# Kernel tuning notes

Hardware: AMD Instinct MI355X
Metric: run time of the kernel (lower is better)

## Reference

```python
import jax, jax.numpy as jnp
import numpy as np

N = 50000
E = 1600000
NFEAT = 256
NHID = 256
PAD_N = 60000


def setup_inputs() -> dict:
    key = jax.random.key(0)
    ks = jax.random.split(key, 8)
    x = jax.random.normal(ks[0], (N, NFEAT), dtype=jnp.float32)
    adj_rows = jax.random.randint(ks[1], (E,), 0, N)
    adj_cols = jax.random.randint(ks[2], (E,), 0, N)
    adj_vals = jax.random.uniform(ks[3], (E,), dtype=jnp.float32)
    pos_idx = jnp.arange(N)  # unique rows within padded output
    W1 = jax.random.normal(ks[4], (NFEAT, NHID), dtype=jnp.float32) * 0.05
    b1 = jax.random.normal(ks[5], (NHID,), dtype=jnp.float32) * 0.05
    W2 = jax.random.normal(ks[6], (NHID, NHID), dtype=jnp.float32) * 0.05
    b2 = jax.random.normal(ks[7], (NHID,), dtype=jnp.float32) * 0.05
    return {"x": x, "adj_rows": adj_rows, "adj_cols": adj_cols,
            "adj_vals": adj_vals, "pad_n": PAD_N, "pos_idx": pos_idx,
            "W1": W1, "b1": b1, "W2": W2, "b2": b2}


def _graph_conv(x, rows, cols, vals, W, b):
    # support = x @ W ; out = adj @ support + b  (adj in COO form)
    support = x @ W                                   # [N, H]
    msgs = vals[:, None] * support[cols]              # [E, H] gather + scale
    agg = jax.ops.segment_sum(msgs, rows, num_segments=x.shape[0])
    return agg + b


def reference(x, adj_rows, adj_cols, adj_vals, pad_n, pos_idx, W1, b1, W2, b2):
    h = jax.nn.relu(_graph_conv(x, adj_rows, adj_cols, adj_vals, W1, b1))
    # dropout: eval mode (training=False) -> identity
    h = jax.nn.relu(_graph_conv(h, adj_rows, adj_cols, adj_vals, W2, b2))
    out = jnp.zeros((pad_n, h.shape[1]), dtype=h.dtype)
    out = out.at[pos_idx].set(h)
    return out
```

## Files before the change

kernel.cpp:

```cpp
#include <hip/hip_runtime.h>
#include <hip/hip_bf16.h>

typedef __attribute__((ext_vector_type(8))) short short8;
typedef __attribute__((ext_vector_type(4))) float f32x4;
typedef __attribute__((ext_vector_type(2))) float f32x2;

#define BUK_SHIFT 7
#define BUK_ROWS 128
#define MAXBUK 400
#define CAP2 6144
#define CHUNK 6250
#define CHUNK_PAD 6272

static __device__ __forceinline__ unsigned short f2bf(float f) {
    unsigned u = __float_as_uint(f);
    u += 0x7fffu + ((u >> 16) & 1u);
    return (unsigned short)(u >> 16);
}
static __device__ __forceinline__ unsigned pk2bf(float a, float b) {
    return (unsigned)f2bf(a) | ((unsigned)f2bf(b) << 16);
}

__global__ void wtr_kernel(const float* __restrict__ W, unsigned short* __restrict__ Wt) {
    int k = blockIdx.x, n = threadIdx.x;
    Wt[n * 256 + k] = f2bf(W[k * 256 + n]);
}


__global__ __launch_bounds__(1024) void bin_count(const int* __restrict__ rows,
                                                  int* __restrict__ cntM, int E, int nbuk) {
    __shared__ int c[MAXBUK];
    for (int i = threadIdx.x; i < nbuk; i += 1024) c[i] = 0;
    __syncthreads();
    int s = blockIdx.x * CHUNK, e = s + CHUNK < E ? s + CHUNK : E;
    for (int i = s + (int)threadIdx.x; i < e; i += 1024) atomicAdd(&c[rows[i] >> BUK_SHIFT], 1);
    __syncthreads();
    for (int i = threadIdx.x; i < nbuk; i += 1024) cntM[i * gridDim.x + blockIdx.x] = c[i];
}

__global__ __launch_bounds__(1024) void scan1_kernel(const int* __restrict__ in,
                                                     int* __restrict__ tmp,
                                                     int* __restrict__ bsum, int n) {
    __shared__ int sdata[1024];
    int i = blockIdx.x * 1024 + threadIdx.x;
    int v = (i < n) ? in[i] : 0;
    sdata[threadIdx.x] = v;
    __syncthreads();
    for (int off = 1; off < 1024; off <<= 1) {
        int t = (threadIdx.x >= (unsigned)off) ? sdata[threadIdx.x - off] : 0;
        __syncthreads();
        sdata[threadIdx.x] += t;
        __syncthreads();
    }
    if (i < n) tmp[i] = sdata[threadIdx.x] - v;
    if (threadIdx.x == 1023) bsum[blockIdx.x] = sdata[1023];
}

__global__ __launch_bounds__(512) void scan2_kernel(const int* __restrict__ bsum,
                                                    int* __restrict__ boff, int nb) {
    __shared__ int s[512];
    int t = threadIdx.x;
    int v = (t < nb) ? bsum[t] : 0;
    s[t] = v;
    __syncthreads();
    for (int off = 1; off < 512; off <<= 1) {
        int x = (t >= off) ? s[t - off] : 0;
        __syncthreads();
        s[t] += x;
        __syncthreads();
    }
    if (t < nb) boff[t] = s[t] - v;
}

__global__ void scan3_kernel(const int* __restrict__ tmp, const int* __restrict__ boff,
                             int* __restrict__ out, int n) {
    int i = blockIdx.x * blockDim.x + threadIdx.x;
    if (i < n) out[i] = tmp[i] + boff[i >> 10];
}

__global__ __launch_bounds__(1024) void bin_scatter(const int* __restrict__ rows,
                                                    const int* __restrict__ cols,
                                                    const float* __restrict__ vals,
                                                    const int* __restrict__ cntS,
                                                    unsigned int* __restrict__ cc,
                                                    unsigned char* __restrict__ rb,
                                                    int E, int nbuk, int nblk) {
    __shared__ unsigned int scc[CHUNK_PAD];
    __shared__ unsigned char srb[CHUNK_PAD];
    __shared__ int lcnt[512], lsc[512], lcur[512];
    const int b = blockIdx.x, tid = threadIdx.x;
    const int s = b * CHUNK, e = s + CHUNK < E ? s + CHUNK : E;
    if (tid < 512) lcnt[tid] = 0;
    __syncthreads();
    for (int i = s + tid; i < e; i += 1024) atomicAdd(&lcnt[rows[i] >> BUK_SHIFT], 1);
    __syncthreads();
    if (tid < 512) lsc[tid] = lcnt[tid];
    __syncthreads();
    for (int off = 1; off < 512; off <<= 1) {
        int t = (tid < 512 && tid >= off) ? lsc[tid - off] : 0;
        __syncthreads();
        if (tid < 512) lsc[tid] += t;
        __syncthreads();
    }
    if (tid < 512) lcur[tid] = lsc[tid] - lcnt[tid];
    __syncthreads();
    for (int i = s + tid; i < e; i += 1024) {
        int r = rows[i];
        int p = atomicAdd(&lcur[r >> BUK_SHIFT], 1);
        scc[p] = ((unsigned)cols[i] << 16) | (unsigned)f2bf(vals[i]);
        srb[p] = (unsigned char)(r & (BUK_ROWS - 1));
    }
    __syncthreads();
    const int wv = tid >> 6, ln = tid & 63;
    for (int bu = wv; bu < nbuk; bu += 16) {
        const int lo = lsc[bu] - lcnt[bu];
        const int n = lcnt[bu];
        const int gbase = cntS[bu * nblk + b];
        for (int j = ln; j < n; j += 64) {
            cc[gbase + j] = scc[lo + j];
            rb[gbase + j] = srb[lo + j];
        }
    }
}

__global__ __launch_bounds__(1024) void bucket_pad(const unsigned int* __restrict__ cc,
                                                   const unsigned char* __restrict__ rb,
                                                   const int* __restrict__ cntS,
                                                   unsigned int* __restrict__ cc2,
                                                   int2* __restrict__ rp,
                                                   int E, int nbuk, int nblk, int N) {
    __shared__ int cnt[BUK_ROWS];
    __shared__ int psc[BUK_ROWS];
    __shared__ int cur[BUK_ROWS];
    const int b = blockIdx.x;
    const int tid = threadIdx.x;
    const int base = cntS[b * nblk];
    const int end = (b + 1 < nbuk) ? cntS[(b + 1) * nblk] : E;
    const int sz = end - base;
    if (tid < BUK_ROWS) cnt[tid] = 0;
    __syncthreads();
    for (int i = tid; i < sz; i += 1024) atomicAdd(&cnt[rb[base + i]], 1);
    __syncthreads();
    if (tid < BUK_ROWS) psc[tid] = (cnt[tid] + 7) & ~7;
    __syncthreads();
    for (int off = 1; off < BUK_ROWS; off <<= 1) {
        int t = (tid < BUK_ROWS && tid >= off) ? psc[tid - off] : 0;
        __syncthreads();
        if (tid < BUK_ROWS) psc[tid] += t;
        __syncthreads();
    }
    if (tid < BUK_ROWS) {
        int c = cnt[tid];
        int pc = (c + 7) & ~7;
        int excl = psc[tid] - pc;
        cur[tid] = excl;
        int st = b * CAP2 + excl;
        rp[b * BUK_ROWS + tid] = make_int2(st, st + pc);
        for (int z = c; z < pc; ++z) cc2[(size_t)st + z] = 0u;
    }
    __syncthreads();
    for (int i = tid; i < sz; i += 1024) {
        int p = atomicAdd(&cur[rb[base + i]], 1);
        cc2[(size_t)b * CAP2 + p] = cc[base + i];
    }
}

template <int AF32>
static __device__ __forceinline__ uint4 load_frag(const char* p) {
    if (AF32) {
        const float* f = (const float*)p;
        float4 f0 = *reinterpret_cast<const float4*>(f);
        float4 f1 = *reinterpret_cast<const float4*>(f + 4);
        uint4 u;
        u.x = pk2bf(f0.x, f0.y); u.y = pk2bf(f0.z, f0.w);
        u.z = pk2bf(f1.x, f1.y); u.w = pk2bf(f1.z, f1.w);
        return u;
    }
    return *reinterpret_cast<const uint4*>(p);
}

template <int AF32>
__global__ __launch_bounds__(256) void gemm_kernel(const void* __restrict__ Av,
                                                   const unsigned short* __restrict__ Bt,
                                                   unsigned char* __restrict__ S8, int M) {
    __shared__ unsigned char lds[2][8192];
    const int esz = AF32 ? 4 : 2;
    const int tid = threadIdx.x;
    const int lane = tid & 63;
    const int wave = tid >> 6;
    const int m0 = blockIdx.x * 64;
    const int l15 = lane & 15;
    const int q = lane >> 4;
    const int sw = (l15 & 7) << 4;

    const int st_r0 = tid >> 3;
    const int st_c = tid & 7;
    const int st_off0 = st_r0 * 128 + ((st_c ^ (st_r0 & 7)) << 4);
    const int st_r1 = st_r0 + 32;
    const int st_off1 = st_r1 * 128 + ((st_c ^ (st_r1 & 7)) << 4);
    int row0 = m0 + st_r0; row0 = row0 < M ? row0 : 0;
    int row1 = m0 + st_r1; row1 = row1 < M ? row1 : 0;
    const char* s0p = (const char*)Av + ((size_t)row0 * 256 + st_c * 8) * esz;
    const char* s1p = (const char*)Av + ((size_t)row1 * 256 + st_c * 8) * esz;

    const unsigned short* bb = Bt + (size_t)(wave * 64 + l15) * 256 + q * 8;

    f32x4 acc[4][4] = {};

    uint4 s0 = load_frag<AF32>(s0p);
    uint4 s1 = load_frag<AF32>(s1p);
    *reinterpret_cast<uint4*>(&lds[0][st_off0]) = s0;
    *reinterpret_cast<uint4*>(&lds[0][st_off1]) = s1;
    __syncthreads();

#pragma unroll
    for (int it = 0; it < 4; ++it) {
        const int buf = it & 1;
        if (it < 3) {
            s0 = load_frag<AF32>(s0p + (size_t)(it + 1) * 64 * esz);
            s1 = load_frag<AF32>(s1p + (size_t)(it + 1) * 64 * esz);
        }
        const int kk = it * 64;
#pragma unroll
        for (int ks = 0; ks < 2; ++ks) {
            short8 a[4], b[4];
#pragma unroll
            for (int mf = 0; mf < 4; ++mf) {
                int r = mf * 16 + l15;
                a[mf] = *reinterpret_cast<const short8*>(
                    &lds[buf][r * 128 + ((ks * 64 + q * 16) ^ sw)]);
            }
#pragma unroll
            for (int nf = 0; nf < 4; ++nf)
                b[nf] = *reinterpret_cast<const short8*>(bb + (size_t)nf * 16 * 256 + kk + ks * 32);
#pragma unroll
            for (int mf = 0; mf < 4; ++mf)
#pragma unroll
                for (int nf = 0; nf < 4; ++nf)
                    acc[mf][nf] = __builtin_amdgcn_mfma_f32_16x16x32_bf16(b[nf], a[mf], acc[mf][nf], 0, 0, 0);
        }
        if (it < 3) {
            *reinterpret_cast<uint4*>(&lds[buf ^ 1][st_off0]) = s0;
            *reinterpret_cast<uint4*>(&lds[buf ^ 1][st_off1]) = s1;
        }
        __syncthreads();
    }

    const int g4 = q * 4;
#pragma unroll
    for (int mf = 0; mf < 4; ++mf) {
        int m = m0 + mf * 16 + l15;
        if (m < M) {
#pragma unroll
            for (int nf = 0; nf < 4; ++nf) {
                int p = __builtin_amdgcn_cvt_pk_fp8_f32(acc[mf][nf][0], acc[mf][nf][1], 0, false);
                p = __builtin_amdgcn_cvt_pk_fp8_f32(acc[mf][nf][2], acc[mf][nf][3], p, true);
                *reinterpret_cast<int*>(S8 + ((size_t)wave * M + m) * 64 + nf * 16 + g4) = p;
            }
        }
    }
}

template <int LAYER2>
__global__ __launch_bounds__(256) void spmm_kernel(const unsigned char* __restrict__ S8,
                                                   const int2* __restrict__ rp,
                                                   const unsigned int* __restrict__ cc,
                                                   const float* __restrict__ bias,
                                                   unsigned short* __restrict__ out_bf,
                                                   float* __restrict__ out_f,
                                                   const int* __restrict__ pos_idx, int N) {
    const int slab = blockIdx.y;
    const int lane = threadIdx.x & 63;
    const int wid = threadIdx.x >> 6;
    const int q = lane >> 4;
    const int l = lane & 15;
    const int row = blockIdx.x * 16 + wid * 4 + q;
    const int2 r = rp[row];
    f32x2 a01 = {0.f, 0.f}, a23 = {0.f, 0.f};
    const unsigned char* Sl = S8 + (size_t)slab * N * 64 + l * 4;
    for (int i = r.x; i < r.y; i += 8) {
        uint4 c0 = *reinterpret_cast<const uint4*>(cc + i);
        uint4 c1 = *reinterpret_cast<const uint4*>(cc + i + 4);
        unsigned w0 = *reinterpret_cast<const unsigned*>(Sl + ((size_t)(c0.x >> 16) << 6));
        unsigned w1 = *reinterpret_cast<const unsigned*>(Sl + ((size_t)(c0.y >> 16) << 6));
        unsigned w2 = *reinterpret_cast<const unsigned*>(Sl + ((size_t)(c0.z >> 16) << 6));
        unsigned w3 = *reinterpret_cast<const unsigned*>(Sl + ((size_t)(c0.w >> 16) << 6));
        unsigned w4 = *reinterpret_cast<const unsigned*>(Sl + ((size_t)(c1.x >> 16) << 6));
        unsigned w5 = *reinterpret_cast<const unsigned*>(Sl + ((size_t)(c1.y >> 16) << 6));
        unsigned w6 = *reinterpret_cast<const unsigned*>(Sl + ((size_t)(c1.z >> 16) << 6));
        unsigned w7 = *reinterpret_cast<const unsigned*>(Sl + ((size_t)(c1.w >> 16) << 6));
        float v0 = __uint_as_float(c0.x << 16), v1 = __uint_as_float(c0.y << 16);
        float v2 = __uint_as_float(c0.z << 16), v3 = __uint_as_float(c0.w << 16);
        float v4 = __uint_as_float(c1.x << 16), v5 = __uint_as_float(c1.y << 16);
        float v6 = __uint_as_float(c1.z << 16), v7 = __uint_as_float(c1.w << 16);
#define ACC(ww, vv) { \
        f32x2 plo = __builtin_amdgcn_cvt_pk_f32_fp8((int)ww, false); \
        f32x2 phi = __builtin_amdgcn_cvt_pk_f32_fp8((int)ww, true);  \
        f32x2 vv2 = {vv, vv}; \
        a01 += vv2 * plo; a23 += vv2 * phi; }
        ACC(w0, v0) ACC(w1, v1) ACC(w2, v2) ACC(w3, v3)
        ACC(w4, v4) ACC(w5, v5) ACC(w6, v6) ACC(w7, v7)
#undef ACC
    }
    if (row >= N) return;
    const int f = slab * 64 + l * 4;
    float a0 = fmaxf(a01.x + bias[f + 0], 0.f);
    float a1 = fmaxf(a01.y + bias[f + 1], 0.f);
    float a2 = fmaxf(a23.x + bias[f + 2], 0.f);
    float a3 = fmaxf(a23.y + bias[f + 3], 0.f);
    if (LAYER2) {
        int orow = pos_idx[row];
        *reinterpret_cast<float4*>(out_f + (size_t)orow * 256 + f) = make_float4(a0, a1, a2, a3);
    } else {
        ushort4 o;
        o.x = f2bf(a0); o.y = f2bf(a1); o.z = f2bf(a2); o.w = f2bf(a3);
        *reinterpret_cast<ushort4*>(out_bf + (size_t)row * 256 + f) = o;
    }
}

extern "C" void kernel_launch(void* const* d_in, const int* in_sizes, int n_in,
                              void* d_out, int out_size, void* d_ws, size_t ws_size,
                              hipStream_t stream) {
    const float* x        = (const float*)d_in[0];
    const int* adj_rows   = (const int*)d_in[1];
    const int* adj_cols   = (const int*)d_in[2];
    const float* adj_vals = (const float*)d_in[3];
    const int* pos_idx    = (const int*)d_in[5];
    const float* W1       = (const float*)d_in[6];
    const float* b1       = (const float*)d_in[7];
    const float* W2       = (const float*)d_in[8];
    const float* b2       = (const float*)d_in[9];

    const int N = in_sizes[0] / 256;
    const int E = in_sizes[1];
    const int nbuk = (N + BUK_ROWS - 1) >> BUK_SHIFT;
    const int nblk = (E + CHUNK - 1) / CHUNK;
    const int n2 = nbuk * nblk;
    const int nb2 = (n2 + 1023) / 1024;
    const int nwork = nbuk * BUK_ROWS;

    char* ws = (char*)d_ws;
    size_t off = 0;
    auto alloc = [&](size_t bytes) {
        char* p = ws + off;
        off += (bytes + 255) & ~(size_t)255;
        return p;
    };
    unsigned short* xb   = (unsigned short*)alloc((size_t)N * 256 * 2);
    unsigned char*  sup8 = (unsigned char*)alloc((size_t)N * 256);
    unsigned short* w1t  = (unsigned short*)alloc(256 * 256 * 2);
    unsigned short* w2t  = (unsigned short*)alloc(256 * 256 * 2);
    int2* rp     = (int2*)alloc((size_t)nwork * 8);
    int* cntM    = (int*)alloc((size_t)n2 * 4);
    int* cntS    = (int*)alloc((size_t)n2 * 4);
    int* tmp     = (int*)alloc((size_t)n2 * 4);
    int* bsum    = (int*)alloc(512 * 4);
    int* boff    = (int*)alloc(512 * 4);
    unsigned int* cc  = (unsigned int*)alloc((size_t)E * 4);
    unsigned char* rb = (unsigned char*)alloc((size_t)E);
    unsigned int* cc2 = (unsigned int*)alloc((size_t)nbuk * CAP2 * 4);
    (void)ws_size; (void)n_in;

    hipMemsetAsync((float*)d_out + (size_t)N * 256, 0,
                   ((size_t)out_size - (size_t)N * 256) * 4, stream);

    wtr_kernel<<<256, 256, 0, stream>>>(W1, w1t);
    wtr_kernel<<<256, 256, 0, stream>>>(W2, w2t);

    bin_count<<<nblk, 1024, 0, stream>>>(adj_rows, cntM, E, nbuk);
    scan1_kernel<<<nb2, 1024, 0, stream>>>(cntM, tmp, bsum, n2);
    scan2_kernel<<<1, 512, 0, stream>>>(bsum, boff, nb2);
    scan3_kernel<<<(n2 + 255) / 256, 256, 0, stream>>>(tmp, boff, cntS, n2);
    bin_scatter<<<nblk, 1024, 0, stream>>>(adj_rows, adj_cols, adj_vals, cntS, cc, rb, E, nbuk, nblk);
    bucket_pad<<<nbuk, 1024, 0, stream>>>(cc, rb, cntS, cc2, rp, E, nbuk, nblk, N);

    const int ggrid = (N + 63) / 64;
    const dim3 sgrid(nwork / 16, 4);
    gemm_kernel<1><<<ggrid, 256, 0, stream>>>(x, w1t, sup8, N);
    spmm_kernel<0><<<sgrid, 256, 0, stream>>>(sup8, rp, cc2, b1, xb, nullptr, nullptr, N);
    gemm_kernel<0><<<ggrid, 256, 0, stream>>>(xb, w2t, sup8, N);
    spmm_kernel<1><<<sgrid, 256, 0, stream>>>(sup8, rp, cc2, b2, nullptr, (float*)d_out, pos_idx, N);
}
```

Measured before the change: 224.8 us.

## Process two feature slabs per SpMM thread, prefetch indices, fuse small setup kernels

The SpMM kernel now handles two 64-column fp8 slabs per thread instead of one and halves the grid's y dimension. Each edge's column index and value are then decoded once and serve two gathers, and the next 8 edges' indices are prefetched while the current batch is processed. Separately, the two weight-transpose launches are merged into one, and the scan3 pass is removed by computing the scanned offsets inline in bin_scatter and bucket_pad. The SpMM change roughly doubles per-thread registers and halves parallelism, and the prefetch reads up to 8 entries past each row's end.

```diff
diff --git a/kernel.cpp b/kernel.cpp
--- a/kernel.cpp
+++ b/kernel.cpp
@@ -21,8 +21,11 @@
     return (unsigned)f2bf(a) | ((unsigned)f2bf(b) << 16);
 }
 
-__global__ void wtr_kernel(const float* __restrict__ W, unsigned short* __restrict__ Wt) {
+__global__ void wtr_kernel(const float* __restrict__ W1, const float* __restrict__ W2,
+                           unsigned short* __restrict__ W1t, unsigned short* __restrict__ W2t) {
     int k = blockIdx.x, n = threadIdx.x;
+    const float* W = blockIdx.y ? W2 : W1;
+    unsigned short* Wt = blockIdx.y ? W2t : W1t;
     Wt[n * 256 + k] = f2bf(W[k * 256 + n]);
 }
 
@@ -72,16 +75,16 @@
     if (t < nb) boff[t] = s[t] - v;
 }
 
-__global__ void scan3_kernel(const int* __restrict__ tmp, const int* __restrict__ boff,
-                             int* __restrict__ out, int n) {
-    int i = blockIdx.x * blockDim.x + threadIdx.x;
-    if (i < n) out[i] = tmp[i] + boff[i >> 10];
+static __device__ __forceinline__ int scanv(const int* __restrict__ tmp,
+                                            const int* __restrict__ boff, int idx) {
+    return tmp[idx] + boff[idx >> 10];
 }
 
 __global__ __launch_bounds__(1024) void bin_scatter(const int* __restrict__ rows,
                                                     const int* __restrict__ cols,
                                                     const float* __restrict__ vals,
-                                                    const int* __restrict__ cntS,
+                                                    const int* __restrict__ tmp,
+                                                    const int* __restrict__ boff,
                                                     unsigned int* __restrict__ cc,
                                                     unsigned char* __restrict__ rb,
                                                     int E, int nbuk, int nblk) {
@@ -115,7 +118,7 @@
     for (int bu = wv; bu < nbuk; bu += 16) {
         const int lo = lsc[bu] - lcnt[bu];
         const int n = lcnt[bu];
-        const int gbase = cntS[bu * nblk + b];
+        const int gbase = scanv(tmp, boff, bu * nblk + b);
         for (int j = ln; j < n; j += 64) {
             cc[gbase + j] = scc[lo + j];
             rb[gbase + j] = srb[lo + j];
@@ -125,7 +128,8 @@
 
 __global__ __launch_bounds__(1024) void bucket_pad(const unsigned int* __restrict__ cc,
                                                    const unsigned char* __restrict__ rb,
-                                                   const int* __restrict__ cntS,
+                                                   const int* __restrict__ tmp,
+                                                   const int* __restrict__ boff,
                                                    unsigned int* __restrict__ cc2,
                                                    int2* __restrict__ rp,
                                                    int E, int nbuk, int nblk, int N) {
@@ -134,8 +138,8 @@
     __shared__ int cur[BUK_ROWS];
     const int b = blockIdx.x;
     const int tid = threadIdx.x;
-    const int base = cntS[b * nblk];
-    const int end = (b + 1 < nbuk) ? cntS[(b + 1) * nblk] : E;
+    const int base = scanv(tmp, boff, b * nblk);
+    const int end = (b + 1 < nbuk) ? scanv(tmp, boff, (b + 1) * nblk) : E;
     const int sz = end - base;
     if (tid < BUK_ROWS) cnt[tid] = 0;
     __syncthreads();
@@ -269,52 +273,67 @@
                                                    unsigned short* __restrict__ out_bf,
                                                    float* __restrict__ out_f,
                                                    const int* __restrict__ pos_idx, int N) {
-    const int slab = blockIdx.y;
+    const int sp = blockIdx.y;
     const int lane = threadIdx.x & 63;
     const int wid = threadIdx.x >> 6;
     const int q = lane >> 4;
     const int l = lane & 15;
     const int row = blockIdx.x * 16 + wid * 4 + q;
     const int2 r = rp[row];
-    f32x2 a01 = {0.f, 0.f}, a23 = {0.f, 0.f};
-    const unsigned char* Sl = S8 + (size_t)slab * N * 64 + l * 4;
-    for (int i = r.x; i < r.y; i += 8) {
+    const unsigned lbyte = (unsigned)l * 4;
+    const unsigned char* __restrict__ SA = S8 + (size_t)(2 * sp) * N * 64;
+    const unsigned char* __restrict__ SB = SA + (size_t)N * 64;
+    f32x2 aA01 = {0.f, 0.f}, aA23 = {0.f, 0.f}, aB01 = {0.f, 0.f}, aB23 = {0.f, 0.f};
+    int i = r.x;
+    if (i < r.y) {
         uint4 c0 = *reinterpret_cast<const uint4*>(cc + i);
         uint4 c1 = *reinterpret_cast<const uint4*>(cc + i + 4);
-        unsigned w0 = *reinterpret_cast<const unsigned*>(Sl + ((size_t)(c0.x >> 16) << 6));
-        unsigned w1 = *reinterpret_cast<const unsigned*>(Sl + ((size_t)(c0.y >> 16) << 6));
-        unsigned w2 = *reinterpret_cast<const unsigned*>(Sl + ((size_t)(c0.z >> 16) << 6));
-        unsigned w3 = *reinterpret_cast<const unsigned*>(Sl + ((size_t)(c0.w >> 16) << 6));
-        unsigned w4 = *reinterpret_cast<const unsigned*>(Sl + ((size_t)(c1.x >> 16) << 6));
-        unsigned w5 = *reinterpret_cast<const unsigned*>(Sl + ((size_t)(c1.y >> 16) << 6));
-        unsigned w6 = *reinterpret_cast<const unsigned*>(Sl + ((size_t)(c1.z >> 16) << 6));
-        unsigned w7 = *reinterpret_cast<const unsigned*>(Sl + ((size_t)(c1.w >> 16) << 6));
-        float v0 = __uint_as_float(c0.x << 16), v1 = __uint_as_float(c0.y << 16);
-        float v2 = __uint_as_float(c0.z << 16), v3 = __uint_as_float(c0.w << 16);
-        float v4 = __uint_as_float(c1.x << 16), v5 = __uint_as_float(c1.y << 16);
-        float v6 = __uint_as_float(c1.z << 16), v7 = __uint_as_float(c1.w << 16);
-#define ACC(ww, vv) { \
-        f32x2 plo = __builtin_amdgcn_cvt_pk_f32_fp8((int)ww, false); \
-        f32x2 phi = __builtin_amdgcn_cvt_pk_f32_fp8((int)ww, true);  \
-        f32x2 vv2 = {vv, vv}; \
-        a01 += vv2 * plo; a23 += vv2 * phi; }
-        ACC(w0, v0) ACC(w1, v1) ACC(w2, v2) ACC(w3, v3)
-        ACC(w4, v4) ACC(w5, v5) ACC(w6, v6) ACC(w7, v7)
-#undef ACC
+        for (; i < r.y; i += 8) {
+            uint4 n0 = *reinterpret_cast<const uint4*>(cc + i + 8);
+            uint4 n1 = *reinterpret_cast<const uint4*>(cc + i + 12);
+            unsigned cw[8] = {c0.x, c0.y, c0.z, c0.w, c1.x, c1.y, c1.z, c1.w};
+            unsigned wA[8], wB[8];
+#pragma unroll
+            for (int e = 0; e < 8; ++e) {
+                unsigned off = ((cw[e] >> 16) << 6) + lbyte;
+                wA[e] = *reinterpret_cast<const unsigned*>(SA + off);
+                wB[e] = *reinterpret_cast<const unsigned*>(SB + off);
+            }
+#pragma unroll
+            for (int e = 0; e < 8; ++e) {
+                float v = __uint_as_float(cw[e] << 16);
+                f32x2 vv = {v, v};
+                aA01 += vv * __builtin_amdgcn_cvt_pk_f32_fp8((int)wA[e], false);
+                aA23 += vv * __builtin_amdgcn_cvt_pk_f32_fp8((int)wA[e], true);
+                aB01 += vv * __builtin_amdgcn_cvt_pk_f32_fp8((int)wB[e], false);
+                aB23 += vv * __builtin_amdgcn_cvt_pk_f32_fp8((int)wB[e], true);
+            }
+            c0 = n0; c1 = n1;
+        }
     }
     if (row >= N) return;
-    const int f = slab * 64 + l * 4;
-    float a0 = fmaxf(a01.x + bias[f + 0], 0.f);
-    float a1 = fmaxf(a01.y + bias[f + 1], 0.f);
-    float a2 = fmaxf(a23.x + bias[f + 2], 0.f);
-    float a3 = fmaxf(a23.y + bias[f + 3], 0.f);
+    const int fA = sp * 128 + l * 4;
+    const int fB = fA + 64;
+    float a0 = fmaxf(aA01.x + bias[fA + 0], 0.f);
+    float a1 = fmaxf(aA01.y + bias[fA + 1], 0.f);
+    float a2 = fmaxf(aA23.x + bias[fA + 2], 0.f);
+    float a3 = fmaxf(aA23.y + bias[fA + 3], 0.f);
+    float b0 = fmaxf(aB01.x + bias[fB + 0], 0.f);
+    float b1 = fmaxf(aB01.y + bias[fB + 1], 0.f);
+    float b2 = fmaxf(aB23.x + bias[fB + 2], 0.f);
+    float b3 = fmaxf(aB23.y + bias[fB + 3], 0.f);
     if (LAYER2) {
         int orow = pos_idx[row];
-        *reinterpret_cast<float4*>(out_f + (size_t)orow * 256 + f) = make_float4(a0, a1, a2, a3);
+        float* o = out_f + (size_t)orow * 256;
+        *reinterpret_cast<float4*>(o + fA) = make_float4(a0, a1, a2, a3);
+        *reinterpret_cast<float4*>(o + fB) = make_float4(b0, b1, b2, b3);
     } else {
-        ushort4 o;
-        o.x = f2bf(a0); o.y = f2bf(a1); o.z = f2bf(a2); o.w = f2bf(a3);
-        *reinterpret_cast<ushort4*>(out_bf + (size_t)row * 256 + f) = o;
+        ushort4 oa, ob;
+        oa.x = f2bf(a0); oa.y = f2bf(a1); oa.z = f2bf(a2); oa.w = f2bf(a3);
+        ob.x = f2bf(b0); ob.y = f2bf(b1); ob.z = f2bf(b2); ob.w = f2bf(b3);
+        unsigned short* o = out_bf + (size_t)row * 256;
+        *reinterpret_cast<ushort4*>(o + fA) = oa;
+        *reinterpret_cast<ushort4*>(o + fB) = ob;
     }
 }
 
@@ -352,7 +371,6 @@
     unsigned short* w2t  = (unsigned short*)alloc(256 * 256 * 2);
     int2* rp     = (int2*)alloc((size_t)nwork * 8);
     int* cntM    = (int*)alloc((size_t)n2 * 4);
-    int* cntS    = (int*)alloc((size_t)n2 * 4);
     int* tmp     = (int*)alloc((size_t)n2 * 4);
     int* bsum    = (int*)alloc(512 * 4);
     int* boff    = (int*)alloc(512 * 4);
@@ -364,18 +382,16 @@
     hipMemsetAsync((float*)d_out + (size_t)N * 256, 0,
                    ((size_t)out_size - (size_t)N * 256) * 4, stream);
 
-    wtr_kernel<<<256, 256, 0, stream>>>(W1, w1t);
-    wtr_kernel<<<256, 256, 0, stream>>>(W2, w2t);
+    wtr_kernel<<<dim3(256, 2), 256, 0, stream>>>(W1, W2, w1t, w2t);
 
     bin_count<<<nblk, 1024, 0, stream>>>(adj_rows, cntM, E, nbuk);
     scan1_kernel<<<nb2, 1024, 0, stream>>>(cntM, tmp, bsum, n2);
     scan2_kernel<<<1, 512, 0, stream>>>(bsum, boff, nb2);
-    scan3_kernel<<<(n2 + 255) / 256, 256, 0, stream>>>(tmp, boff, cntS, n2);
-    bin_scatter<<<nblk, 1024, 0, stream>>>(adj_rows, adj_cols, adj_vals, cntS, cc, rb, E, nbuk, nblk);
-    bucket_pad<<<nbuk, 1024, 0, stream>>>(cc, rb, cntS, cc2, rp, E, nbuk, nblk, N);
+    bin_scatter<<<nblk, 1024, 0, stream>>>(adj_rows, adj_cols, adj_vals, tmp, boff, cc, rb, E, nbuk, nblk);
+    bucket_pad<<<nbuk, 1024, 0, stream>>>(cc, rb, tmp, boff, cc2, rp, E, nbuk, nblk, N);
 
     const int ggrid = (N + 63) / 64;
-    const dim3 sgrid(nwork / 16, 4);
+    const dim3 sgrid(nwork / 16, 2);
     gemm_kernel<1><<<ggrid, 256, 0, stream>>>(x, w1t, sup8, N);
     spmm_kernel<0><<<sgrid, 256, 0, stream>>>(sup8, rp, cc2, b1, xb, nullptr, nullptr, N);
     gemm_kernel<0><<<ggrid, 256, 0, stream>>>(xb, w2t, sup8, N);
```

Result: slower. 245.6 us (+9.3%).
